# Kernel optimization log

Hardware: AMD Instinct MI355X
Metric: run time of the kernel (lower is better)

Reference implementation:

```python
import jax, jax.numpy as jnp
import numpy as np

B, S = 4, 4096
VOCAB = 32000
HIDDEN = 2048
INT_DIM = 64
N_LC = 8192


def _gelu(x):
    # torch nn.GELU() default is the exact (erf) formulation
    return jax.nn.gelu(x, approximate=False)


def setup_inputs() -> dict:
    key = jax.random.key(0)
    ks = jax.random.split(key, 12)
    inp = {
        "input_ids": jax.random.randint(ks[0], (B, S), 0, VOCAB, dtype=jnp.int64) if jax.config.jax_enable_x64 else jax.random.randint(ks[0], (B, S), 0, VOCAB, dtype=jnp.int32),
        "lc_values": jax.random.normal(ks[1], (N_LC, 1), dtype=jnp.float32),
        "pos_b": jax.random.randint(ks[2], (N_LC,), 0, B, dtype=jnp.int32),
        "pos_s": jax.random.randint(ks[3], (N_LC,), 0, S, dtype=jnp.int32),
        # learned params
        "wte": jax.random.normal(ks[4], (VOCAB, HIDDEN), dtype=jnp.float32) * 0.02,
        "W0": jax.random.normal(ks[5], (1, INT_DIM), dtype=jnp.float32) * 0.5,
        "b0": jnp.zeros((INT_DIM,), dtype=jnp.float32),
        "W1": jax.random.normal(ks[6], (INT_DIM, INT_DIM), dtype=jnp.float32) * (1.0 / np.sqrt(INT_DIM)),
        "b1": jnp.zeros((INT_DIM,), dtype=jnp.float32),
        "W2": jax.random.normal(ks[7], (INT_DIM, INT_DIM), dtype=jnp.float32) * (1.0 / np.sqrt(INT_DIM)),
        "b2": jnp.zeros((INT_DIM,), dtype=jnp.float32),
        "Wout": jax.random.normal(ks[8], (INT_DIM, HIDDEN), dtype=jnp.float32) * (1.0 / np.sqrt(INT_DIM)),
        "bout": jnp.zeros((HIDDEN,), dtype=jnp.float32),
    }
    return inp


def reference(input_ids, lc_values, pos_b, pos_s, wte, W0, b0, W1, b1, W2, b2, Wout, bout):
    V = wte.shape[0]
    # clamp_min(0).clamp_max(vocab_size); clip to V-1 so the gather is in-range
    ids = jnp.clip(input_ids, 0, V - 1)
    hidden = wte[ids]  # [B, S, H] embedding gather
    h = lc_values @ W0 + b0
    h = _gelu(h) @ W1 + b1
    h = _gelu(h) @ W2 + b2
    lc_features = _gelu(h) @ Wout + bout  # [N_lc, H]
    # index_put(..., accumulate=False): overwrite rows at (pos_b, pos_s)
    return hidden.at[pos_b, pos_s].set(lc_features.astype(hidden.dtype))
```

## Files before the change

### kernel.cpp

```cpp
#include <hip/hip_runtime.h>
#include <hip/hip_bf16.h>
#include <math.h>

#define BB 4
#define SS 4096
#define HH 2048
#define VOCAB 32000
#define NLC 8192
#define ROWS (BB*SS)

#define FROWS 32
#define FCOLS 512

__device__ __forceinline__ float gelu_exact(float x) {
    return 0.5f * x * (1.0f + erff(x * 0.70710678118654752f));
}

__global__ void scatter_win_kernel(const int* __restrict__ pos_b, const int* __restrict__ pos_s,
                                   int* __restrict__ win) {
    int i = blockIdx.x * blockDim.x + threadIdx.x;
    if (i < NLC) {
        int p = pos_b[i] * SS + pos_s[i];
        atomicMax(&win[p], i + 1);
    }
}

__global__ void mlp_g2_kernel(const float* __restrict__ lc, const float* __restrict__ W0,
                              const float* __restrict__ b0, const float* __restrict__ W1,
                              const float* __restrict__ b1, const float* __restrict__ W2,
                              const float* __restrict__ b2, float* __restrict__ g2out) {
    int w = threadIdx.x >> 6;
    int j = threadIdx.x & 63;
    int row = blockIdx.x * 4 + w;
    __shared__ float g[4][64];
    float x = lc[row];
    float h = gelu_exact(fmaf(x, W0[j], b0[j]));
    g[w][j] = h;
    __syncthreads();
    float acc = b1[j];
#pragma unroll
    for (int k = 0; k < 64; ++k) acc = fmaf(g[w][k], W1[k * 64 + j], acc);
    acc = gelu_exact(acc);
    __syncthreads();
    g[w][j] = acc;
    __syncthreads();
    float acc2 = b2[j];
#pragma unroll
    for (int k = 0; k < 64; ++k) acc2 = fmaf(g[w][k], W2[k * 64 + j], acc2);
    g2out[row * 64 + j] = gelu_exact(acc2);
}

__global__ void feat_scatter_kernel(const float* __restrict__ g2, const int* __restrict__ win,
                                    const int* __restrict__ pos_b, const int* __restrict__ pos_s,
                                    const float* __restrict__ Wout, const float* __restrict__ bout,
                                    float* __restrict__ out) {
    __shared__ float g2s[FROWS][64];
    __shared__ int   wrow[FROWS];
    int t = threadIdx.x;
    int rblk = blockIdx.x & 255;
    int cb   = (blockIdx.x >> 8) * FCOLS;
    int base = rblk * FROWS;

    {
        const float4* src = (const float4*)(g2 + base * 64);
        float4* dst = (float4*)&g2s[0][0];
        dst[t] = src[t];
        dst[t + 256] = src[t + 256];
    }
    if (t < FROWS) {
        int i = base + t;
        int p = pos_b[i] * SS + pos_s[i];
        wrow[t] = (win[p] == i + 1) ? p : -1;
    }
    __syncthreads();

    int w = t >> 6, l = t & 63;
    const float* wbase = Wout + cb + l * 4;

    float4 bv0 = *(const float4*)&bout[cb + l * 4];
    float4 bv1 = *(const float4*)&bout[cb + 256 + l * 4];
    float4 acc0[8], acc1[8];
#pragma unroll
    for (int r = 0; r < 8; ++r) { acc0[r] = bv0; acc1[r] = bv1; }

    for (int k0 = 0; k0 < 64; k0 += 4) {
        float4 wv0[4], wv1[4];
#pragma unroll
        for (int kk = 0; kk < 4; ++kk) {
            const float* wp = wbase + (size_t)(k0 + kk) * HH;
            wv0[kk] = *(const float4*)wp;
            wv1[kk] = *(const float4*)(wp + 256);
        }
#pragma unroll
        for (int r = 0; r < 8; ++r) {
            float4 gv = *(const float4*)&g2s[w * 8 + r][k0];
#pragma unroll
            for (int c = 0; c < 4; ++c) {
                float g0 = (&gv.x)[0], g1 = (&gv.x)[1], g2v = (&gv.x)[2], g3 = (&gv.x)[3];
                (&acc0[r].x)[c] = fmaf(g0, (&wv0[0].x)[c],
                                  fmaf(g1, (&wv0[1].x)[c],
                                  fmaf(g2v, (&wv0[2].x)[c],
                                  fmaf(g3, (&wv0[3].x)[c], (&acc0[r].x)[c]))));
                (&acc1[r].x)[c] = fmaf(g0, (&wv1[0].x)[c],
                                  fmaf(g1, (&wv1[1].x)[c],
                                  fmaf(g2v, (&wv1[2].x)[c],
                                  fmaf(g3, (&wv1[3].x)[c], (&acc1[r].x)[c]))));
            }
        }
    }

#pragma unroll
    for (int r = 0; r < 8; ++r) {
        int p = wrow[w * 8 + r];
        if (p < 0) continue;
        float* op = out + (size_t)p * HH + cb + l * 4;
        *(float4*)op = acc0[r];
        *(float4*)(op + 256) = acc1[r];
    }
}

__global__ void gather_kernel(const int* __restrict__ ids, const int* __restrict__ win,
                              const float* __restrict__ wte, float* __restrict__ out) {
    int row = blockIdx.x;
    if (win[row] != 0) return;
    int id = ids[row];
    id = id < 0 ? 0 : (id > VOCAB - 1 ? VOCAB - 1 : id);
    const float4* src = (const float4*)(wte + (size_t)id * HH);
    float4* dst = (float4*)(out + (size_t)row * HH);
    for (int e = threadIdx.x; e < HH / 4; e += 256) dst[e] = src[e];
}

extern "C" void kernel_launch(void* const* d_in, const int* in_sizes, int n_in,
                              void* d_out, int out_size, void* d_ws, size_t ws_size,
                              hipStream_t stream) {
    const int*   ids  = (const int*)d_in[0];
    const float* lc   = (const float*)d_in[1];
    const int*   pb   = (const int*)d_in[2];
    const int*   ps   = (const int*)d_in[3];
    const float* wte  = (const float*)d_in[4];
    const float* W0   = (const float*)d_in[5];
    const float* b0   = (const float*)d_in[6];
    const float* W1   = (const float*)d_in[7];
    const float* b1   = (const float*)d_in[8];
    const float* W2   = (const float*)d_in[9];
    const float* b2   = (const float*)d_in[10];
    const float* Wout = (const float*)d_in[11];
    const float* bout = (const float*)d_in[12];
    float* out = (float*)d_out;

    int*   win = (int*)d_ws;
    float* g2  = (float*)((char*)d_ws + ROWS * sizeof(int));

    hipMemsetAsync(win, 0, ROWS * sizeof(int), stream);
    scatter_win_kernel<<<NLC / 256, 256, 0, stream>>>(pb, ps, win);
    mlp_g2_kernel<<<NLC / 4, 256, 0, stream>>>(lc, W0, b0, W1, b1, W2, b2, g2);
    feat_scatter_kernel<<<(NLC / FROWS) * (HH / FCOLS), 256, 0, stream>>>(g2, win, pb, ps, Wout, bout, out);
    gather_kernel<<<ROWS, 256, 0, stream>>>(ids, win, wte, out);
}
```

Before: 422.7 us.

## Fuse scatter-win into MLP kernel and gather into feature kernel

Merges the winner-index atomic scatter into the MLP kernel, so the first blocks also do the atomics. Merges the embedding gather into the feature-projection kernel as extra blocks, cutting the launch count from four to two. The gather now uses nontemporal stores so the large output write does not pollute the cache. Feature and gather blocks can now run concurrently, with the risk of mixed-block imbalance within one grid.

```diff
diff --git a/kernel.cpp b/kernel.cpp
--- a/kernel.cpp
+++ b/kernel.cpp
@@ -11,26 +11,29 @@
 
 #define FROWS 32
 #define FCOLS 512
+#define FEAT_BLOCKS ((NLC / FROWS) * (HH / FCOLS))
+
+typedef float fvec4 __attribute__((ext_vector_type(4)));
 
 __device__ __forceinline__ float gelu_exact(float x) {
     return 0.5f * x * (1.0f + erff(x * 0.70710678118654752f));
 }
 
-__global__ void scatter_win_kernel(const int* __restrict__ pos_b, const int* __restrict__ pos_s,
+__global__ void mlp_scatter_kernel(const float* __restrict__ lc, const float* __restrict__ W0,
+                                   const float* __restrict__ b0, const float* __restrict__ W1,
+                                   const float* __restrict__ b1, const float* __restrict__ W2,
+                                   const float* __restrict__ b2, float* __restrict__ g2out,
+                                   const int* __restrict__ pos_b, const int* __restrict__ pos_s,
                                    int* __restrict__ win) {
-    int i = blockIdx.x * blockDim.x + threadIdx.x;
-    if (i < NLC) {
+    int t = threadIdx.x;
+    if (blockIdx.x < NLC / 256) {
+        int i = blockIdx.x * 256 + t;
         int p = pos_b[i] * SS + pos_s[i];
         atomicMax(&win[p], i + 1);
     }
-}
 
-__global__ void mlp_g2_kernel(const float* __restrict__ lc, const float* __restrict__ W0,
-                              const float* __restrict__ b0, const float* __restrict__ W1,
-                              const float* __restrict__ b1, const float* __restrict__ W2,
-                              const float* __restrict__ b2, float* __restrict__ g2out) {
-    int w = threadIdx.x >> 6;
-    int j = threadIdx.x & 63;
+    int w = t >> 6;
+    int j = t & 63;
     int row = blockIdx.x * 4 + w;
     __shared__ float g[4][64];
     float x = lc[row];
@@ -50,13 +53,29 @@
     g2out[row * 64 + j] = gelu_exact(acc2);
 }
 
-__global__ void feat_scatter_kernel(const float* __restrict__ g2, const int* __restrict__ win,
-                                    const int* __restrict__ pos_b, const int* __restrict__ pos_s,
-                                    const float* __restrict__ Wout, const float* __restrict__ bout,
-                                    float* __restrict__ out) {
+__global__ void feat_gather_kernel(const float* __restrict__ g2, const int* __restrict__ win,
+                                   const int* __restrict__ pos_b, const int* __restrict__ pos_s,
+                                   const float* __restrict__ Wout, const float* __restrict__ bout,
+                                   const int* __restrict__ ids, const float* __restrict__ wte,
+                                   float* __restrict__ out) {
     __shared__ float g2s[FROWS][64];
     __shared__ int   wrow[FROWS];
     int t = threadIdx.x;
+
+    if (blockIdx.x >= FEAT_BLOCKS) {
+        int row = blockIdx.x - FEAT_BLOCKS;
+        if (win[row] > 0) return;
+        int id = ids[row];
+        id = id < 0 ? 0 : (id > VOCAB - 1 ? VOCAB - 1 : id);
+        const fvec4* src = (const fvec4*)(wte + (size_t)id * HH);
+        fvec4* dst = (fvec4*)(out + (size_t)row * HH);
+        fvec4 v0 = src[t];
+        fvec4 v1 = src[t + 256];
+        __builtin_nontemporal_store(v0, &dst[t]);
+        __builtin_nontemporal_store(v1, &dst[t + 256]);
+        return;
+    }
+
     int rblk = blockIdx.x & 255;
     int cb   = (blockIdx.x >> 8) * FCOLS;
     int base = rblk * FROWS;
@@ -119,17 +138,6 @@
     }
 }
 
-__global__ void gather_kernel(const int* __restrict__ ids, const int* __restrict__ win,
-                              const float* __restrict__ wte, float* __restrict__ out) {
-    int row = blockIdx.x;
-    if (win[row] != 0) return;
-    int id = ids[row];
-    id = id < 0 ? 0 : (id > VOCAB - 1 ? VOCAB - 1 : id);
-    const float4* src = (const float4*)(wte + (size_t)id * HH);
-    float4* dst = (float4*)(out + (size_t)row * HH);
-    for (int e = threadIdx.x; e < HH / 4; e += 256) dst[e] = src[e];
-}
-
 extern "C" void kernel_launch(void* const* d_in, const int* in_sizes, int n_in,
                               void* d_out, int out_size, void* d_ws, size_t ws_size,
                               hipStream_t stream) {
@@ -151,9 +159,7 @@
     int*   win = (int*)d_ws;
     float* g2  = (float*)((char*)d_ws + ROWS * sizeof(int));
 
-    hipMemsetAsync(win, 0, ROWS * sizeof(int), stream);
-    scatter_win_kernel<<<NLC / 256, 256, 0, stream>>>(pb, ps, win);
-    mlp_g2_kernel<<<NLC / 4, 256, 0, stream>>>(lc, W0, b0, W1, b1, W2, b2, g2);
-    feat_scatter_kernel<<<(NLC / FROWS) * (HH / FCOLS), 256, 0, stream>>>(g2, win, pb, ps, Wout, bout, out);
-    gather_kernel<<<ROWS, 256, 0, stream>>>(ids, win, wte, out);
+    (void)hipMemsetAsync(win, 0, ROWS * sizeof(int), stream);
+    mlp_scatter_kernel<<<NLC / 4, 256, 0, stream>>>(lc, W0, b0, W1, b1, W2, b2, g2, pb, ps, win);
+    feat_gather_kernel<<<FEAT_BLOCKS + ROWS, 256, 0, stream>>>(g2, win, pb, ps, Wout, bout, ids, wte, out);
 }
```

After: 412.3 us. 2.5% less time.
